# Optimization experiments

Measured on AMD Instinct MI355X. Metric: run time of the kernel, lower is better.

## Reference

```python
import jax, jax.numpy as jnp
import numpy as np
from jax import lax

B, C_IN, C_OUT, L, K, PAD = 4, 16, 16, 1024, 5, 2


def setup_inputs() -> dict:
    key = jax.random.key(0)
    k1, k2 = jax.random.split(key)
    scores = jax.random.normal(k1, (B, C_IN, L, L), dtype=jnp.float32)
    # kaiming_uniform_(a=sqrt(5)) -> bound = 1/sqrt(fan_in), fan_in = (C_IN/groups)*K*K
    fan_in = C_IN * K * K
    bound = 1.0 / np.sqrt(fan_in)
    weight = jax.random.uniform(k2, (C_OUT, C_IN, K, K), dtype=jnp.float32,
                                minval=-bound, maxval=bound)
    bias = jnp.zeros((C_OUT,), dtype=jnp.float32)
    return {"scores": scores, "weight": weight, "bias": bias}


def reference(scores, weight, bias):
    # scores: [B, C_in, L, L]
    Lq = scores.shape[-2]
    causal = jnp.tril(jnp.ones((Lq, Lq), dtype=bool))  # [L, L]
    # mask_{-inf} then softmax over key dim
    masked = jnp.where(causal, scores, -jnp.inf)
    probs = jax.nn.softmax(masked, axis=-1)
    # grouped conv2d over the [L, L] score map (shape-preserving padding)
    out = lax.conv_general_dilated(
        probs, weight,
        window_strides=(1, 1),
        padding=((PAD, PAD), (PAD, PAD)),
        rhs_dilation=(1, 1),
        dimension_numbers=("NCHW", "OIHW", "NCHW"),
        feature_group_count=1,
    )
    out = out + bias[None, :, None, None]
    # mask_{0}: zero out non-causal positions
    out = jnp.where(causal, out, jnp.zeros((), dtype=out.dtype))
    return out
```

## Files before the change

### kernel.cpp

```cpp
#include <hip/hip_runtime.h>
#include <hip/hip_bf16.h>
#include <math.h>

#define LSEQ  1024
#define CIN   16
#define COUT  16
#define BATCH 4
#define TILE  16
#define NT    13
#define CSTR  48
#define RSTR  (20 * CSTR)

typedef __attribute__((ext_vector_type(8))) short short8;
typedef __attribute__((ext_vector_type(4))) float f32x4;

static __device__ __forceinline__ unsigned short f2bf(float f) {
    unsigned u = __builtin_bit_cast(unsigned, f);
    u += 0x7fff + ((u >> 16) & 1);
    return (unsigned short)(u >> 16);
}

__global__ __launch_bounds__(256) void stats_kernel(const float* __restrict__ scores,
                                                    float* __restrict__ rowinv)
{
    const int w   = blockIdx.x;
    const int row = w & (LSEQ - 1);
    const int tid = threadIdx.x;
    const int j0  = tid * 4;
    float4 v = make_float4(0.f, 0.f, 0.f, 0.f);
    if (j0 <= row) v = *(const float4*)(scores + (size_t)w * LSEQ + j0);
    float s = 0.f;
    s += (j0 + 0 <= row) ? __expf(v.x) : 0.f;
    s += (j0 + 1 <= row) ? __expf(v.y) : 0.f;
    s += (j0 + 2 <= row) ? __expf(v.z) : 0.f;
    s += (j0 + 3 <= row) ? __expf(v.w) : 0.f;
    #pragma unroll
    for (int off = 32; off > 0; off >>= 1) s += __shfl_xor(s, off, 64);
    __shared__ float part[4];
    if ((tid & 63) == 0) part[tid >> 6] = s;
    __syncthreads();
    if (tid == 0) rowinv[w] = 1.0f / (part[0] + part[1] + part[2] + part[3]);
}

__global__ void wprep_kernel(const float* __restrict__ weight, ushort* __restrict__ wfrag)
{
    const int lane = threadIdx.x;
    const int co   = lane & 15;
    const int q    = lane >> 4;
    const int ci0  = (q & 1) * 8;
    const int cb   = q >> 1;
    for (int t = 0; t < NT; ++t) {
        const int c = 2 * t + cb;
        ushort* dst = wfrag + (size_t)(t * 64 + lane) * 8;
        #pragma unroll
        for (int jj = 0; jj < 8; ++jj) {
            float wv = (c < 25) ? weight[co * (CIN * 25) + (ci0 + jj) * 25 + c] : 0.f;
            dst[jj] = f2bf(wv);
        }
    }
}

__global__ __launch_bounds__(256) void conv_mfma_kernel(
    const float* __restrict__ scores,
    const float* __restrict__ bias,
    const float* __restrict__ rowinv,
    const ushort* __restrict__ wfrag,
    float* __restrict__ out)
{
    const int jt = blockIdx.x, it = blockIdx.y, b = blockIdx.z;
    const int j0 = jt * TILE, i0 = it * TILE;
    const int tid = threadIdx.x;

    if (jt > it) {
        #pragma unroll
        for (int vv = 0; vv < 4; ++vv) {
            int e  = vv * 256 + tid;
            int co = e >> 6, il = (e >> 2) & 15, jq = e & 3;
            *(float4*)(out + ((size_t)(b * COUT + co) * LSEQ + i0 + il) * LSEQ + j0 + jq * 4)
                = make_float4(0.f, 0.f, 0.f, 0.f);
        }
        return;
    }

    const int lane = tid & 63;
    const int w    = tid >> 6;
    const int n    = lane & 15;
    const int q    = lane >> 4;

    short8 af[NT];
    #pragma unroll
    for (int t = 0; t < NT; ++t)
        af[t] = *(const short8*)(wfrag + (size_t)(t * 64 + lane) * 8);

    float bs[4];
    #pragma unroll
    for (int r = 0; r < 4; ++r) bs[r] = bias[q * 4 + r];

    int addr[NT];
    {
        const int cb  = q >> 1;
        const int cio = (q & 1) * 16;
        #pragma unroll
        for (int t = 0; t < NT; ++t) {
            int c = 2 * t + cb;
            if (c >= 25) addr[t] = 0;
            else {
                int kh = c / 5, kw = c - kh * 5;
                addr[t] = (kh * 20 + (n + kw)) * CSTR + cio + w * (4 * RSTR);
            }
        }
    }

    __shared__ ushort ptile[20 * 20 * 24];

    for (int u = 0; u < 8; ++u) {
        int e = u * 256 + tid;
        if (e < 1920) {
            int ci  = e / 120;
            int rem = e - ci * 120;
            int rr  = rem / 6;
            int cq  = rem - rr * 6;
            int row  = i0 - 2 + rr;
            int gcol = j0 - 4 + cq * 4;
            bool rok = (row >= 0) && (row < LSEQ);
            float rinv = 0.f;
            float4 v = make_float4(0.f, 0.f, 0.f, 0.f);
            if (rok) {
                int rid = (b * CIN + ci) * LSEQ + row;
                rinv = rowinv[rid];
                if (gcol >= 0 && gcol <= LSEQ - 4 && gcol <= row)
                    v = *(const float4*)(scores + (size_t)rid * LSEQ + gcol);
            }
            float pv[4] = {v.x, v.y, v.z, v.w};
            #pragma unroll
            for (int l = 0; l < 4; ++l) {
                int col = gcol + l;
                int cc  = cq * 4 - 2 + l;
                bool ok = rok && col >= 0 && col < LSEQ && col <= row;
                float p = ok ? __expf(pv[l]) * rinv : 0.f;
                if (cc >= 0 && cc < 20)
                    ptile[(rr * 20 + cc) * 24 + ci] = f2bf(p);
            }
        }
    }
    __syncthreads();

    #pragma unroll
    for (int s = 0; s < 4; ++s) {
        f32x4 acc = {0.f, 0.f, 0.f, 0.f};
        #pragma unroll
        for (int t = 0; t < NT; ++t) {
            short8 bf = *(const short8*)((const char*)ptile + addr[t] + s * RSTR);
            acc = __builtin_amdgcn_mfma_f32_16x16x32_bf16(af[t], bf, acc, 0, 0, 0);
        }
        const int il = w * 4 + s;
        const int i  = i0 + il;
        const int j  = j0 + n;
        #pragma unroll
        for (int r = 0; r < 4; ++r) {
            const int co = q * 4 + r;
            float val = (j <= i) ? (acc[r] + bs[r]) : 0.f;
            out[((size_t)(b * COUT + co) * LSEQ + i) * LSEQ + j] = val;
        }
    }
}

extern "C" void kernel_launch(void* const* d_in, const int* in_sizes, int n_in,
                              void* d_out, int out_size, void* d_ws, size_t ws_size,
                              hipStream_t stream) {
    const float* scores = (const float*)d_in[0];
    const float* weight = (const float*)d_in[1];
    const float* bias   = (const float*)d_in[2];
    float* out = (float*)d_out;

    float*  rowinv = (float*)d_ws;
    ushort* wfrag  = (ushort*)((char*)d_ws + (size_t)BATCH * CIN * LSEQ * 4);

    stats_kernel<<<BATCH * CIN * LSEQ, 256, 0, stream>>>(scores, rowinv);
    wprep_kernel<<<1, 64, 0, stream>>>(weight, wfrag);

    dim3 g(LSEQ / TILE, LSEQ / TILE, BATCH);
    conv_mfma_kernel<<<g, 256, 0, stream>>>(scores, bias, rowinv, wfrag, out);
}
```

Measured before the change: 559.3 us.

## Materialize bf16 softmax probabilities in workspace and feed conv from them

A new first pass computes each causal row's softmax in a single wave, keeping the exponentials in registers, and writes bf16 probabilities to a 128MB workspace buffer. The weight-fragment prep is folded into an extra block of the same launch. The conv kernel then fills its tile from the bf16 probabilities instead of re-reading fp32 scores and recomputing exp for the halo in every tile. This trades the scores re-read and redundant exp work for an extra bf16 write and read, plus gather loads that pull one 2-byte value from each of eight channel planes. The new path runs only when the workspace is large enough; otherwise the old three-kernel path is kept as a fallback.

```diff
diff --git a/kernel.cpp b/kernel.cpp
--- a/kernel.cpp
+++ b/kernel.cpp
@@ -11,17 +11,178 @@
 #define CSTR  48
 #define RSTR  (20 * CSTR)
 
+#define WFRAG_BYTES (NT * 64 * 8 * 2)
+#define PROBS_ELEMS ((size_t)BATCH * CIN * LSEQ * LSEQ)
+#define WS_NEEDED   (WFRAG_BYTES + PROBS_ELEMS * 2)
+
 typedef __attribute__((ext_vector_type(8))) short short8;
 typedef __attribute__((ext_vector_type(4))) float f32x4;
-
-static __device__ __forceinline__ unsigned short f2bf(float f) {
+typedef __attribute__((ext_vector_type(4))) int   i32x4;
+
+static __device__ __forceinline__ unsigned f2bf_u(float f) {
     unsigned u = __builtin_bit_cast(unsigned, f);
-    u += 0x7fff + ((u >> 16) & 1);
-    return (unsigned short)(u >> 16);
-}
-
-__global__ __launch_bounds__(256) void stats_kernel(const float* __restrict__ scores,
-                                                    float* __restrict__ rowinv)
+    return (u + 0x7fff + ((u >> 16) & 1)) >> 16;
+}
+static __device__ __forceinline__ unsigned short f2bf(float f) { return (unsigned short)f2bf_u(f); }
+
+__global__ __launch_bounds__(256) void softmax_probs_kernel(
+    const float* __restrict__ scores,
+    const float* __restrict__ weight,
+    ushort* __restrict__ wfrag,
+    ushort* __restrict__ probs)
+{
+    const int tid = threadIdx.x;
+
+    if (blockIdx.x == (BATCH * CIN * LSEQ / 4)) {
+        for (int slot = tid; slot < NT * 64; slot += 256) {
+            const int t = slot >> 6, lane = slot & 63;
+            const int co = lane & 15, q = lane >> 4;
+            const int ci0 = (q & 1) * 8, cb = q >> 1;
+            const int c = 2 * t + cb;
+            ushort* dst = wfrag + (size_t)slot * 8;
+            #pragma unroll
+            for (int jj = 0; jj < 8; ++jj) {
+                float wv = (c < 25) ? weight[co * (CIN * 25) + (ci0 + jj) * 25 + c] : 0.f;
+                dst[jj] = f2bf(wv);
+            }
+        }
+        return;
+    }
+
+    const int w    = blockIdx.x * 4 + (tid >> 6);
+    const int lane = tid & 63;
+    const int i    = w & (LSEQ - 1);
+    const float* rowp = scores + (size_t)w * LSEQ;
+
+    float e[16];
+    #pragma unroll
+    for (int c = 0; c < 4; ++c) {
+        const int j0 = c * 256 + lane * 4;
+        float4 v = make_float4(0.f, 0.f, 0.f, 0.f);
+        if (c * 256 <= i) v = *(const float4*)(rowp + j0);
+        e[c*4+0] = (j0 + 0 <= i) ? __expf(v.x) : 0.f;
+        e[c*4+1] = (j0 + 1 <= i) ? __expf(v.y) : 0.f;
+        e[c*4+2] = (j0 + 2 <= i) ? __expf(v.z) : 0.f;
+        e[c*4+3] = (j0 + 3 <= i) ? __expf(v.w) : 0.f;
+    }
+    float s = 0.f;
+    #pragma unroll
+    for (int t = 0; t < 16; ++t) s += e[t];
+    #pragma unroll
+    for (int off = 32; off > 0; off >>= 1) s += __shfl_xor(s, off, 64);
+    const float rinv = 1.0f / s;
+
+    ushort* prow = probs + (size_t)w * LSEQ;
+    #pragma unroll
+    for (int c = 0; c < 4; ++c) {
+        if (c * 256 <= i) {
+            const int j0 = c * 256 + lane * 4;
+            uint2 pk;
+            pk.x = f2bf_u(e[c*4+0] * rinv) | (f2bf_u(e[c*4+1] * rinv) << 16);
+            pk.y = f2bf_u(e[c*4+2] * rinv) | (f2bf_u(e[c*4+3] * rinv) << 16);
+            *(uint2*)(prow + j0) = pk;
+        }
+    }
+}
+
+__global__ __launch_bounds__(256) void conv_mfma2_kernel(
+    const ushort* __restrict__ probs,
+    const float* __restrict__ bias,
+    const ushort* __restrict__ wfrag,
+    float* __restrict__ out)
+{
+    const int jt = blockIdx.x, it = blockIdx.y, b = blockIdx.z;
+    const int j0 = jt * TILE, i0 = it * TILE;
+    const int tid = threadIdx.x;
+
+    if (jt > it) {
+        #pragma unroll
+        for (int vv = 0; vv < 4; ++vv) {
+            int e  = vv * 256 + tid;
+            int co = e >> 6, il = (e >> 2) & 15, jq = e & 3;
+            *(float4*)(out + ((size_t)(b * COUT + co) * LSEQ + i0 + il) * LSEQ + j0 + jq * 4)
+                = make_float4(0.f, 0.f, 0.f, 0.f);
+        }
+        return;
+    }
+
+    const int lane = tid & 63;
+    const int w    = tid >> 6;
+    const int n    = lane & 15;
+    const int q    = lane >> 4;
+
+    short8 af[NT];
+    #pragma unroll
+    for (int t = 0; t < NT; ++t)
+        af[t] = *(const short8*)(wfrag + (size_t)(t * 64 + lane) * 8);
+
+    float bs[4];
+    #pragma unroll
+    for (int r = 0; r < 4; ++r) bs[r] = bias[q * 4 + r];
+
+    int addr[NT];
+    {
+        const int cb  = q >> 1;
+        const int cio = (q & 1) * 16;
+        #pragma unroll
+        for (int t = 0; t < NT; ++t) {
+            int c = 2 * t + cb;
+            if (c >= 25) addr[t] = 0;
+            else {
+                int kh = c / 5, kw = c - kh * 5;
+                addr[t] = (kh * 20 + (n + kw)) * CSTR + cio + w * (4 * RSTR);
+            }
+        }
+    }
+
+    __shared__ ushort ptile[20 * 20 * 24];
+
+    const ushort* pb = probs + (size_t)b * CIN * LSEQ * LSEQ;
+    #pragma unroll
+    for (int u = 0; u < 4; ++u) {
+        const int e = u * 256 + tid;
+        if (e < 800) {
+            const int half = e & 1, cell = e >> 1;
+            const int rr = cell / 20, cc = cell - rr * 20;
+            const int row = i0 - 2 + rr;
+            const int col = j0 - 2 + cc;
+            const bool ok = (row >= 0) && (row < LSEQ) && (col >= 0) && (col < LSEQ) && (col <= row);
+            const size_t base = ok ? ((size_t)row * LSEQ + col + (size_t)half * 8 * LSEQ * LSEQ) : 0;
+            unsigned uu[8];
+            #pragma unroll
+            for (int k = 0; k < 8; ++k)
+                uu[k] = pb[base + (size_t)k * LSEQ * LSEQ];
+            i32x4 pk;
+            #pragma unroll
+            for (int k = 0; k < 4; ++k) {
+                unsigned v = uu[2*k] | (uu[2*k+1] << 16);
+                pk[k] = ok ? (int)v : 0;
+            }
+            *(i32x4*)((char*)ptile + cell * CSTR + half * 16) = pk;
+        }
+    }
+    __syncthreads();
+
+    #pragma unroll
+    for (int s = 0; s < 4; ++s) {
+        f32x4 acc = {0.f, 0.f, 0.f, 0.f};
+        #pragma unroll
+        for (int t = 0; t < NT; ++t) {
+            short8 bf = *(const short8*)((const char*)ptile + addr[t] + s * RSTR);
+            acc = __builtin_amdgcn_mfma_f32_16x16x32_bf16(af[t], bf, acc, 0, 0, 0);
+        }
+        const int i = i0 + w * 4 + s;
+        const int j = j0 + n;
+        #pragma unroll
+        for (int r = 0; r < 4; ++r) {
+            const int co = q * 4 + r;
+            out[((size_t)(b * COUT + co) * LSEQ + i) * LSEQ + j] = (j <= i) ? (acc[r] + bs[r]) : 0.f;
+        }
+    }
+}
+
+__global__ __launch_bounds__(256) void stats_fb_kernel(const float* __restrict__ scores,
+                                                       float* __restrict__ rowinv)
 {
     const int w   = blockIdx.x;
     const int row = w & (LSEQ - 1);
@@ -42,7 +203,7 @@
     if (tid == 0) rowinv[w] = 1.0f / (part[0] + part[1] + part[2] + part[3]);
 }
 
-__global__ void wprep_kernel(const float* __restrict__ weight, ushort* __restrict__ wfrag)
+__global__ void wprep_fb_kernel(const float* __restrict__ weight, ushort* __restrict__ wfrag)
 {
     const int lane = threadIdx.x;
     const int co   = lane & 15;
@@ -60,7 +221,7 @@
     }
 }
 
-__global__ __launch_bounds__(256) void conv_mfma_kernel(
+__global__ __launch_bounds__(256) void conv_fb_kernel(
     const float* __restrict__ scores,
     const float* __restrict__ bias,
     const float* __restrict__ rowinv,
@@ -153,14 +314,12 @@
             short8 bf = *(const short8*)((const char*)ptile + addr[t] + s * RSTR);
             acc = __builtin_amdgcn_mfma_f32_16x16x32_bf16(af[t], bf, acc, 0, 0, 0);
         }
-        const int il = w * 4 + s;
-        const int i  = i0 + il;
-        const int j  = j0 + n;
+        const int i = i0 + w * 4 + s;
+        const int j = j0 + n;
         #pragma unroll
         for (int r = 0; r < 4; ++r) {
             const int co = q * 4 + r;
-            float val = (j <= i) ? (acc[r] + bs[r]) : 0.f;
-            out[((size_t)(b * COUT + co) * LSEQ + i) * LSEQ + j] = val;
+            out[((size_t)(b * COUT + co) * LSEQ + i) * LSEQ + j] = (j <= i) ? (acc[r] + bs[r]) : 0.f;
         }
     }
 }
@@ -173,12 +332,23 @@
     const float* bias   = (const float*)d_in[2];
     float* out = (float*)d_out;
 
-    float*  rowinv = (float*)d_ws;
-    ushort* wfrag  = (ushort*)((char*)d_ws + (size_t)BATCH * CIN * LSEQ * 4);
-
-    stats_kernel<<<BATCH * CIN * LSEQ, 256, 0, stream>>>(scores, rowinv);
-    wprep_kernel<<<1, 64, 0, stream>>>(weight, wfrag);
-
-    dim3 g(LSEQ / TILE, LSEQ / TILE, BATCH);
-    conv_mfma_kernel<<<g, 256, 0, stream>>>(scores, bias, rowinv, wfrag, out);
-}
+    if (ws_size >= WS_NEEDED) {
+        ushort* wfrag = (ushort*)d_ws;
+        ushort* probs = (ushort*)((char*)d_ws + WFRAG_BYTES);
+
+        softmax_probs_kernel<<<BATCH * CIN * LSEQ / 4 + 1, 256, 0, stream>>>(
+            scores, weight, wfrag, probs);
+
+        dim3 g(LSEQ / TILE, LSEQ / TILE, BATCH);
+        conv_mfma2_kernel<<<g, 256, 0, stream>>>(probs, bias, wfrag, out);
+    } else {
+        float*  rowinv = (float*)d_ws;
+        ushort* wfrag  = (ushort*)((char*)d_ws + (size_t)BATCH * CIN * LSEQ * 4);
+
+        stats_fb_kernel<<<BATCH * CIN * LSEQ, 256, 0, stream>>>(scores, rowinv);
+        wprep_fb_kernel<<<1, 64, 0, stream>>>(weight, wfrag);
+
+        dim3 g(LSEQ / TILE, LSEQ / TILE, BATCH);
+        conv_fb_kernel<<<g, 256, 0, stream>>>(scores, bias, rowinv, wfrag, out);
+    }
+}
```

After: 555.9 us. Within noise of the previous version (-0.6%).
